# Optimization experiments

Hardware: AMD Instinct MI355X
Metric: run time of the kernel (lower is better)

Reference implementation:

```python
import jax, jax.numpy as jnp
import numpy as np

EPS = 1e-5
K = 3
N_TAP = K * K


def _bn(x, g, b, m, v):
    # eval-mode batchnorm over channel axis 1 of NCHW
    inv = g / jnp.sqrt(v + EPS)
    return x * inv[None, :, None, None] + (b - m * inv)[None, :, None, None]


def _silu(x):
    return x * jax.nn.sigmoid(x)


def _dcn(x, offset, mask, w, b, pad=1):
    """Modulated deformable conv (DCNv2), stride 1.
    x: [B,C,H,W], offset: [B,2n,H,W] ((dy,dx) per tap), mask: [B,n,H,W],
    w: [O,C,K,K], b: [O]."""
    B, C, H, W = x.shape
    O = w.shape[0]
    ky, kx = jnp.meshgrid(jnp.arange(K), jnp.arange(K), indexing='ij')
    ky = ky.reshape(N_TAP).astype(x.dtype)
    kx = kx.reshape(N_TAP).astype(x.dtype)
    off = offset.reshape(B, N_TAP, 2, H, W)
    base_y = jnp.arange(H, dtype=x.dtype)[None, None, :, None]
    base_x = jnp.arange(W, dtype=x.dtype)[None, None, None, :]
    # fractional sample positions [B,n,H,W]
    py = base_y - pad + ky[None, :, None, None] + off[:, :, 0]
    px = base_x - pad + kx[None, :, None, None] + off[:, :, 1]
    y0 = jnp.floor(py)
    x0 = jnp.floor(px)
    fy = py - y0
    fx = px - x0
    y0i = y0.astype(jnp.int32)
    x0i = x0.astype(jnp.int32)
    x_flat = x.reshape(B, C, 1, H * W)

    def corner(yi, xi, wgt):
        valid = (yi >= 0) & (yi < H) & (xi >= 0) & (xi < W)
        idx = (jnp.clip(yi, 0, H - 1) * W + jnp.clip(xi, 0, W - 1)).reshape(B, 1, N_TAP, H * W)
        v = jnp.take_along_axis(x_flat, idx, axis=-1)  # [B,C,n,HW]
        return v * (wgt * valid.astype(x.dtype)).reshape(B, 1, N_TAP, H * W)

    acc = corner(y0i, x0i, (1 - fy) * (1 - fx))
    acc = acc + corner(y0i, x0i + 1, (1 - fy) * fx)
    acc = acc + corner(y0i + 1, x0i, fy * (1 - fx))
    acc = acc + corner(y0i + 1, x0i + 1, fy * fx)
    val = acc.reshape(B, C, N_TAP, H, W) * mask[:, None]  # modulation
    out = jnp.einsum('bcnhw,ocn->bohw', val, w.reshape(O, C, N_TAP))
    return out + b[None, :, None, None]


def setup_inputs() -> dict:
    key = jax.random.key(0)
    ks = jax.random.split(key, 16)
    B, C1, H, W = 8, 256, 80, 80
    C2 = 256
    Ch = 128  # c_ = int(c2 * 0.5)
    d = {}
    d['x'] = jax.random.normal(ks[0], (B, C1, H, W), jnp.float32)
    # cv1: 1x1 conv (no bias) + BN
    d['cv1_w'] = jax.random.normal(ks[1], (Ch, C1), jnp.float32) * (1.0 / np.sqrt(C1))
    d['bn1_g'] = jax.random.uniform(ks[2], (Ch,), jnp.float32, 0.5, 1.5)
    d['bn1_b'] = jax.random.normal(ks[3], (Ch,), jnp.float32) * 0.1
    d['bn1_m'] = jax.random.normal(ks[4], (Ch,), jnp.float32) * 0.1
    d['bn1_v'] = jax.random.uniform(ks[5], (Ch,), jnp.float32, 0.5, 1.5)
    # offset/mask predictor 3x3 conv (small weights -> modest deformation)
    d['off_w'] = jax.random.normal(ks[6], (3 * N_TAP, Ch, K, K), jnp.float32) * 0.01
    d['off_b'] = jnp.zeros((3 * N_TAP,), jnp.float32)
    # dcn main weight/bias
    d['dcn_w'] = jax.random.normal(ks[7], (Ch, Ch, K, K), jnp.float32) * (1.0 / np.sqrt(Ch * N_TAP))
    d['dcn_b'] = jnp.zeros((Ch,), jnp.float32)
    d['bn2_g'] = jax.random.uniform(ks[8], (Ch,), jnp.float32, 0.5, 1.5)
    d['bn2_b'] = jax.random.normal(ks[9], (Ch,), jnp.float32) * 0.1
    d['bn2_m'] = jax.random.normal(ks[10], (Ch,), jnp.float32) * 0.1
    d['bn2_v'] = jax.random.uniform(ks[11], (Ch,), jnp.float32, 0.5, 1.5)
    # cv2: 1x1 conv (no bias) + BN
    d['cv2_w'] = jax.random.normal(ks[12], (C2, Ch), jnp.float32) * (1.0 / np.sqrt(Ch))
    d['bn3_g'] = jax.random.uniform(ks[13], (C2,), jnp.float32, 0.5, 1.5)
    d['bn3_b'] = jax.random.normal(ks[14], (C2,), jnp.float32) * 0.1
    d['bn3_m'] = jax.random.normal(ks[15], (C2,), jnp.float32) * 0.1
    d['bn3_v'] = jnp.ones((C2,), jnp.float32)
    return d


def reference(x, cv1_w, bn1_g, bn1_b, bn1_m, bn1_v,
              off_w, off_b, dcn_w, dcn_b, bn2_g, bn2_b, bn2_m, bn2_v,
              cv2_w, bn3_g, bn3_b, bn3_m, bn3_v):
    # cv1: 1x1 conv -> BN -> SiLU
    y = _silu(_bn(jnp.einsum('bchw,oc->bohw', x, cv1_w), bn1_g, bn1_b, bn1_m, bn1_v))
    # offset/mask predictor: 3x3 conv, pad 1
    raw = jax.lax.conv_general_dilated(
        y, off_w, window_strides=(1, 1), padding=((1, 1), (1, 1)),
        dimension_numbers=('NCHW', 'OIHW', 'NCHW')) + off_b[None, :, None, None]
    offset = raw[:, :2 * N_TAP]
    mask = jax.nn.sigmoid(raw[:, 2 * N_TAP:])
    # modulated deformable 3x3 conv -> BN -> SiLU
    y = _silu(_bn(_dcn(y, offset, mask, dcn_w, dcn_b), bn2_g, bn2_b, bn2_m, bn2_v))
    # cv2: 1x1 conv -> BN -> SiLU
    y = _silu(_bn(jnp.einsum('bchw,oc->bohw', y, cv2_w), bn3_g, bn3_b, bn3_m, bn3_v))
    return x + y  # shortcut (c1 == c2)
```

## Files before the change

kernel.cpp:

```cpp
#include <hip/hip_runtime.h>
#include <math.h>

#define HWSZ 6400
#define WIMG 80
#define HIMG 80
#define BEPS 1e-5f

typedef __attribute__((ext_vector_type(8))) short short8;
typedef __attribute__((ext_vector_type(4))) float f32x4;
typedef __attribute__((ext_vector_type(4))) unsigned u32x4;

__device__ __forceinline__ unsigned short f2b(float f) {
    unsigned u = __builtin_bit_cast(unsigned, f);
    u += 0x7fffu + ((u >> 16) & 1u);
    return (unsigned short)(u >> 16);
}
__device__ __forceinline__ float silu_f(float t) { return t / (1.f + __expf(-t)); }

#define BMFMA(a, b, c) __builtin_amdgcn_mfma_f32_16x16x32_bf16(a, b, c, 0, 0, 0)

__device__ __forceinline__ void gload16(const unsigned short* g, unsigned short* l) {
    __builtin_amdgcn_global_load_lds(
        (const __attribute__((address_space(1))) unsigned int*)g,
        (__attribute__((address_space(3))) unsigned int*)l, 16, 0, 0);
}

__global__ __launch_bounds__(256) void k_prep(
    const float* __restrict__ cv1w, const float* __restrict__ g1, const float* __restrict__ b1,
    const float* __restrict__ m1, const float* __restrict__ v1,
    const float* __restrict__ offw, const float* __restrict__ offb,
    const float* __restrict__ dcnw, const float* __restrict__ dcnb,
    const float* __restrict__ g2, const float* __restrict__ b2,
    const float* __restrict__ m2, const float* __restrict__ v2,
    const float* __restrict__ cv2w, const float* __restrict__ g3, const float* __restrict__ b3,
    const float* __restrict__ m3, const float* __restrict__ v3,
    unsigned short* __restrict__ apk1, unsigned short* __restrict__ apko,
    unsigned short* __restrict__ apkd, unsigned short* __restrict__ apk2,
    float* __restrict__ bias1, float* __restrict__ biaso,
    float* __restrict__ bias2, float* __restrict__ bias3)
{
    int idx = blockIdx.x * 256 + threadIdx.x;
    if (idx < 32768) {
        int j = idx & 7, L = (idx >> 3) & 63, ks = (idx >> 9) & 7, mt = idx >> 12;
        int o = mt * 16 + (L & 15), k = ks * 32 + (L >> 4) * 8 + j;
        float inv = g1[o] * rsqrtf(v1[o] + BEPS);
        apk1[idx] = f2b(cv1w[o * 256 + k] * inv);
    } else if (idx < 69632) {
        int t = idx - 32768;
        int j = t & 7, L = (t >> 3) & 63;
        int mt = t / 18432, rem = t % 18432, ks = rem >> 9;
        int o = mt * 16 + (L & 15);
        int kp = ks * 32 + (L >> 4) * 8 + j;
        int n = kp >> 7, c = kp & 127;
        float wv = (o < 27) ? offw[(size_t)(o * 128 + c) * 9 + n] : 0.f;
        apko[((size_t)(ks * 2 + mt) * 64 + L) * 8 + j] = f2b(wv);
    } else if (idx < 217088) {
        int t = idx - 69632;
        int j = t & 7, L = (t >> 3) & 63;
        int mt = t / 18432, rem = t % 18432, ks = rem >> 9;
        int o = mt * 16 + (L & 15);
        int kp = ks * 32 + (L >> 4) * 8 + j;
        int n = kp >> 7, c = kp & 127;
        float inv = g2[o] * rsqrtf(v2[o] + BEPS);
        apkd[((size_t)(ks * 8 + mt) * 64 + L) * 8 + j] = f2b(dcnw[(size_t)(o * 128 + c) * 9 + n] * inv);
    } else if (idx < 249856) {
        int t = idx - 217088;
        int j = t & 7, L = (t >> 3) & 63, ks = (t >> 9) & 3, mt = t >> 11;
        int o = mt * 16 + (L & 15), k = ks * 32 + (L >> 4) * 8 + j;
        float inv = g3[o] * rsqrtf(v3[o] + BEPS);
        apk2[((size_t)(ks * 16 + mt) * 64 + L) * 8 + j] = f2b(cv2w[o * 128 + k] * inv);
    } else if (idx < 250395) {
        int t = idx - 249856;
        if (t < 128) { float inv = g1[t] * rsqrtf(v1[t] + BEPS); bias1[t] = b1[t] - m1[t] * inv; }
        else if (t < 155) { biaso[t - 128] = offb[t - 128]; }
        else if (t < 283) { int o = t - 155; float inv = g2[o] * rsqrtf(v2[o] + BEPS);
                            bias2[o] = dcnb[o] * inv + b2[o] - m2[o] * inv; }
        else { int o = t - 283; float inv = g3[o] * rsqrtf(v3[o] + BEPS); bias3[o] = b3[o] - m3[o] * inv; }
    }
}

__global__ __launch_bounds__(256) void k_cv1(
    const float* __restrict__ x, const unsigned short* __restrict__ apk1,
    const float* __restrict__ bias1, unsigned short* __restrict__ y1t)
{
    __shared__ __align__(16) unsigned short sB[20480];
    int blk = blockIdx.x;
    int b = blk / 100, pt = blk % 100;
    int p0 = pt * 64;
    int tid = threadIdx.x;
    int lane = tid & 63;
    int w = tid >> 6;
    {
        int px = lane, q = w;
        const float* xb = x + (size_t)b * 256 * HWSZ + p0 + px;
        for (int ks = 0; ks < 8; ++ks) {
            unsigned pk[4];
#pragma unroll
            for (int t = 0; t < 4; ++t) {
                float f0 = xb[(size_t)(ks * 32 + q * 8 + 2 * t) * HWSZ];
                float f1 = xb[(size_t)(ks * 32 + q * 8 + 2 * t + 1) * HWSZ];
                asm("v_cvt_pk_bf16_f32 %0, %1, %2" : "=v"(pk[t]) : "v"(f0), "v"(f1));
            }
            *(u32x4*)&sB[((ks * 4 + (px >> 4)) * 16 + (px & 15)) * 40 + q * 8] =
                (u32x4){pk[0], pk[1], pk[2], pk[3]};
        }
    }
    __syncthreads();
    int n16 = lane & 15, qd = lane >> 4;
    f32x4 acc[2][4];
#pragma unroll
    for (int mi = 0; mi < 2; ++mi)
#pragma unroll
        for (int nt = 0; nt < 4; ++nt) acc[mi][nt] = (f32x4){0.f, 0.f, 0.f, 0.f};
    for (int ks = 0; ks < 8; ++ks) {
        short8 bf[4];
#pragma unroll
        for (int nt = 0; nt < 4; ++nt)
            bf[nt] = *(const short8*)&sB[((ks * 4 + nt) * 16 + n16) * 40 + qd * 8];
        short8 a0 = *(const short8*)&apk1[(size_t)(((w * 2 + 0) * 8 + ks) * 64 + lane) * 8];
        short8 a1 = *(const short8*)&apk1[(size_t)(((w * 2 + 1) * 8 + ks) * 64 + lane) * 8];
#pragma unroll
        for (int nt = 0; nt < 4; ++nt) acc[0][nt] = BMFMA(a0, bf[nt], acc[0][nt]);
#pragma unroll
        for (int nt = 0; nt < 4; ++nt) acc[1][nt] = BMFMA(a1, bf[nt], acc[1][nt]);
    }
    __syncthreads();
#pragma unroll
    for (int mi = 0; mi < 2; ++mi)
#pragma unroll
        for (int nt = 0; nt < 4; ++nt)
#pragma unroll
            for (int r = 0; r < 4; ++r) {
                int o = w * 32 + mi * 16 + qd * 4 + r;
                float sv = silu_f(acc[mi][nt][r] + bias1[o]);
                sB[(nt * 16 + n16) * 136 + o] = f2b(sv);
            }
    __syncthreads();
    {
        int px = tid >> 2, qq = tid & 3;
        unsigned short* ytb = y1t + ((size_t)b * HWSZ + p0 + px) * 128;
#pragma unroll
        for (int seg = 0; seg < 4; ++seg) {
            short8 v = *(const short8*)&sB[px * 136 + qq * 32 + seg * 8];
            *(short8*)&ytb[qq * 32 + seg * 8] = v;
        }
    }
}

#define HY2 8
#define HX2 20
#define NH 160
#define NSLAB 53

#define ACC8(uu, cb)                                                                   \
    {                                                                                  \
        _Pragma("unroll") for (int t = 0; t < 4; ++t) {                                \
            unsigned uv = (uu)[t];                                                     \
            av[(cb) + 2 * t] = fmaf(wk, __builtin_bit_cast(float, uv << 16),           \
                                    av[(cb) + 2 * t]);                                 \
            av[(cb) + 2 * t + 1] = fmaf(wk, __builtin_bit_cast(float, uv & 0xffff0000u),\
                                        av[(cb) + 2 * t + 1]);                         \
        }                                                                              \
    }

__device__ __forceinline__ const unsigned short* slab_src(
    const unsigned short* apko, const unsigned short* apkd,
    const unsigned short* apk2, int i) {
    if (i < 9)  return apko + (size_t)i * 4096;
    if (i < 45) return apkd + (size_t)(i - 9) * 4096;
    return apk2 + (size_t)(i - 45) * 4096;
}

#define STAGE(i, bp)                                                                   \
    {                                                                                  \
        const unsigned short* src_ = slab_src(apko, apkd, apk2, (i));                  \
        gload16(src_ + ((w * 2 + 0) * 512 + lane * 8), &sAf[bp][(w * 2 + 0) * 512]);   \
        gload16(src_ + ((w * 2 + 1) * 512 + lane * 8), &sAf[bp][(w * 2 + 1) * 512]);   \
    }

__global__ __launch_bounds__(256, 2) void k_odc(
    const unsigned short* __restrict__ y1t,
    const unsigned short* __restrict__ apko, const float* __restrict__ biaso,
    const unsigned short* __restrict__ apkd, const float* __restrict__ bias2,
    const unsigned short* __restrict__ apk2, const float* __restrict__ bias3,
    const float* __restrict__ x, float* __restrict__ out)
{
    __shared__ __align__(16) unsigned short sH[NH * 128];
    __shared__ float sRaw[27 * 66];
    __shared__ __align__(16) unsigned short sAf[2][4096];

    int blk = blockIdx.x;
    int b = blk / 100, pt = blk % 100;
    int h0 = (pt / 5) * 4, w0 = (pt % 5) * 16;
    int tid = threadIdx.x, lane = tid & 63, w = tid >> 6;
    int n16 = lane & 15, qd = lane >> 4;
    int pxl = w * 16 + n16;
    const unsigned short* yb = y1t + (size_t)b * HWSZ * 128;

    for (int i = tid; i < NH * 16; i += 256) {
        int r = i >> 4, u = i & 15;
        int ly = r / HX2, lx = r % HX2;
        int yy = min(max(h0 + ly - 2, 0), HIMG - 1);
        int xx = min(max(w0 + lx - 2, 0), WIMG - 1);
        *(u32x4*)&sH[r * 128 + ((u ^ (r & 7)) * 8)] =
            *(const u32x4*)&yb[(size_t)(yy * WIMG + xx) * 128 + u * 8];
    }
    STAGE(0, 0)
    __syncthreads();
    int bufp = 0;

    {
        f32x4 oa0 = (f32x4){0.f, 0.f, 0.f, 0.f};
        f32x4 oa1 = (f32x4){0.f, 0.f, 0.f, 0.f};
        for (int n = 0; n < 9; ++n) {
            STAGE(n + 1, bufp ^ 1)
            int dh = n / 3 - 1, dw = n % 3 - 1;
            int hh = h0 + w + dh, ww = w0 + n16 + dw;
            bool valid = ((unsigned)hh < HIMG) && ((unsigned)ww < WIMG);
            int r = (w + 2 + dh) * HX2 + (n16 + 2 + dw);
            int xr = r & 7;
            const unsigned short* hb = &sH[r * 128];
#pragma unroll
            for (int s = 0; s < 4; ++s) {
                short8 bf = *(const short8*)&hb[((s * 4 + qd) ^ xr) * 8];
                if (!valid) bf = (short8){0, 0, 0, 0, 0, 0, 0, 0};
                short8 a0 = *(const short8*)&sAf[bufp][(s * 2 + 0) * 512 + lane * 8];
                short8 a1 = *(const short8*)&sAf[bufp][(s * 2 + 1) * 512 + lane * 8];
                oa0 = BMFMA(a0, bf, oa0);
                oa1 = BMFMA(a1, bf, oa1);
            }
            if (n == 8) {
#pragma unroll
                for (int mi = 0; mi < 2; ++mi)
#pragma unroll
                    for (int r4 = 0; r4 < 4; ++r4) {
                        int o = mi * 16 + qd * 4 + r4;
                        if (o < 27) {
                            float t = (mi ? oa1[r4] : oa0[r4]) + biaso[o];
                            if (o >= 18) t = 1.f / (1.f + __expf(-t));
                            sRaw[o * 66 + pxl] = t;
                        }
                    }
            }
            __syncthreads();
            bufp ^= 1;
        }
    }

    f32x4 acc[8];
#pragma unroll
    for (int mt = 0; mt < 8; ++mt) acc[mt] = (f32x4){0.f, 0.f, 0.f, 0.f};
    int hI = h0 + w, wI = w0 + n16;

    for (int n = 0; n < 9; ++n) {
        float av[32];
#pragma unroll
        for (int s = 0; s < 4; ++s) {
            int slab = 9 + n * 4 + s;
            if (slab + 1 < NSLAB) STAGE(slab + 1, bufp ^ 1)
            if (s == 0) {
                float dy = sRaw[(2 * n) * 66 + pxl];
                float dx = sRaw[(2 * n + 1) * 66 + pxl];
                float mk = sRaw[(18 + n) * 66 + pxl];
                float py = (float)(hI - 1 + n / 3) + dy;
                float px = (float)(wI - 1 + n % 3) + dx;
                float y0f = floorf(py), x0f = floorf(px);
                float fy = py - y0f, fxv = px - x0f;
                int y0 = (int)y0f, x0 = (int)x0f;
                float wy0 = (1.f - fy) * mk, wy1 = fy * mk, fx1 = 1.f - fxv;
#pragma unroll
                for (int j = 0; j < 32; ++j) av[j] = 0.f;
#pragma unroll
                for (int k = 0; k < 4; ++k) {
                    int yy = y0 + (k >> 1), xx = x0 + (k & 1);
                    bool vld = ((unsigned)yy < HIMG) && ((unsigned)xx < WIMG);
                    float wk = ((k >> 1) ? wy1 : wy0) * ((k & 1) ? fxv : fx1);
                    if (!vld) wk = 0.f;
                    int yc = min(max(yy, 0), HIMG - 1);
                    int xc = min(max(xx, 0), WIMG - 1);
                    int ly = yc - h0 + 2, lx = xc - w0 + 2;
                    if (((unsigned)ly < HY2) && ((unsigned)lx < HX2)) {
                        int r = ly * HX2 + lx;
                        const unsigned short* hb = &sH[r * 128];
                        int xr = r & 7;
                        u32x4 u0 = *(const u32x4*)&hb[((0 + qd) ^ xr) * 8];
                        u32x4 u1 = *(const u32x4*)&hb[((4 + qd) ^ xr) * 8];
                        u32x4 u2 = *(const u32x4*)&hb[((8 + qd) ^ xr) * 8];
                        u32x4 u3 = *(const u32x4*)&hb[((12 + qd) ^ xr) * 8];
                        ACC8(u0, 0) ACC8(u1, 8) ACC8(u2, 16) ACC8(u3, 24)
                    } else if (wk != 0.f) {
                        const unsigned short* src = &yb[(size_t)(yc * WIMG + xc) * 128 + qd * 8];
                        u32x4 u0 = *(const u32x4*)src;
                        u32x4 u1 = *(const u32x4*)(src + 32);
                        u32x4 u2 = *(const u32x4*)(src + 64);
                        u32x4 u3 = *(const u32x4*)(src + 96);
                        ACC8(u0, 0) ACC8(u1, 8) ACC8(u2, 16) ACC8(u3, 24)
                    }
                }
            }
            unsigned pk0, pk1, pk2, pk3;
            asm("v_cvt_pk_bf16_f32 %0, %1, %2" : "=v"(pk0) : "v"(av[s * 8 + 0]), "v"(av[s * 8 + 1]));
            asm("v_cvt_pk_bf16_f32 %0, %1, %2" : "=v"(pk1) : "v"(av[s * 8 + 2]), "v"(av[s * 8 + 3]));
            asm("v_cvt_pk_bf16_f32 %0, %1, %2" : "=v"(pk2) : "v"(av[s * 8 + 4]), "v"(av[s * 8 + 5]));
            asm("v_cvt_pk_bf16_f32 %0, %1, %2" : "=v"(pk3) : "v"(av[s * 8 + 6]), "v"(av[s * 8 + 7]));
            short8 bfv = __builtin_bit_cast(short8, (u32x4){pk0, pk1, pk2, pk3});
#pragma unroll
            for (int mt = 0; mt < 8; ++mt) {
                short8 af = *(const short8*)&sAf[bufp][mt * 512 + lane * 8];
                acc[mt] = BMFMA(af, bfv, acc[mt]);
            }
            if (n == 8 && s == 3) {
                unsigned short* sE = sH;
#pragma unroll
                for (int mt = 0; mt < 8; ++mt)
#pragma unroll
                    for (int r4 = 0; r4 < 4; ++r4) {
                        int o = mt * 16 + qd * 4 + r4;
                        float sv = silu_f(acc[mt][r4] + bias2[o]);
                        sE[pxl * 136 + o] = f2b(sv);
                    }
            }
            __syncthreads();
            bufp ^= 1;
        }
    }

    const unsigned short* sE = sH;
    f32x4 c2[16];
#pragma unroll
    for (int mt = 0; mt < 16; ++mt) c2[mt] = (f32x4){0.f, 0.f, 0.f, 0.f};
#pragma unroll
    for (int h2 = 0; h2 < 8; ++h2) {
        int slab = 45 + h2;
        if (slab + 1 < NSLAB) STAGE(slab + 1, bufp ^ 1)
        int ks = h2 >> 1, half = h2 & 1;
        short8 bf = *(const short8*)&sE[pxl * 136 + ks * 32 + qd * 8];
#pragma unroll
        for (int mt = 0; mt < 8; ++mt) {
            short8 af = *(const short8*)&sAf[bufp][mt * 512 + lane * 8];
            c2[half * 8 + mt] = BMFMA(af, bf, c2[half * 8 + mt]);
        }
        __syncthreads();
        bufp ^= 1;
    }
    int p = (h0 + w) * WIMG + w0 + n16;
    const float* xb = x + (size_t)b * 256 * HWSZ;
    float* ob = out + (size_t)b * 256 * HWSZ;
#pragma unroll
    for (int mt = 0; mt < 16; ++mt)
#pragma unroll
        for (int r4 = 0; r4 < 4; ++r4) {
            int o = mt * 16 + qd * 4 + r4;
            size_t idx = (size_t)o * HWSZ + p;
            ob[idx] = xb[idx] + silu_f(c2[mt][r4] + bias3[o]);
        }
}

extern "C" void kernel_launch(void* const* d_in, const int* in_sizes, int n_in,
                              void* d_out, int out_size, void* d_ws, size_t ws_size,
                              hipStream_t stream) {
    const float* x     = (const float*)d_in[0];
    const float* cv1w  = (const float*)d_in[1];
    const float* bn1g  = (const float*)d_in[2];
    const float* bn1b  = (const float*)d_in[3];
    const float* bn1m  = (const float*)d_in[4];
    const float* bn1v  = (const float*)d_in[5];
    const float* offw  = (const float*)d_in[6];
    const float* offb  = (const float*)d_in[7];
    const float* dcnw  = (const float*)d_in[8];
    const float* dcnb  = (const float*)d_in[9];
    const float* bn2g  = (const float*)d_in[10];
    const float* bn2b  = (const float*)d_in[11];
    const float* bn2m  = (const float*)d_in[12];
    const float* bn2v  = (const float*)d_in[13];
    const float* cv2w  = (const float*)d_in[14];
    const float* bn3g  = (const float*)d_in[15];
    const float* bn3b  = (const float*)d_in[16];
    const float* bn3m  = (const float*)d_in[17];
    const float* bn3v  = (const float*)d_in[18];
    float* out = (float*)d_out;

    float* base = (float*)d_ws;
    unsigned short* y1t = (unsigned short*)base;
    unsigned short* apk1 = (unsigned short*)(base + 7936000);
    unsigned short* apko = (unsigned short*)(base + 7952384);
    unsigned short* apkd = (unsigned short*)(base + 7970816);
    unsigned short* apk2 = (unsigned short*)(base + 8044544);
    float* bias1 = base + 8060928;
    float* biaso = base + 8061056;
    float* bias2 = base + 8061088;
    float* bias3 = base + 8061216;

    k_prep<<<979, 256, 0, stream>>>(cv1w, bn1g, bn1b, bn1m, bn1v,
                                    offw, offb, dcnw, dcnb,
                                    bn2g, bn2b, bn2m, bn2v,
                                    cv2w, bn3g, bn3b, bn3m, bn3v,
                                    apk1, apko, apkd, apk2,
                                    bias1, biaso, bias2, bias3);
    k_cv1<<<800, 256, 0, stream>>>(x, apk1, bias1, y1t);
    k_odc<<<800, 256, 0, stream>>>(y1t, apko, biaso, apkd, bias2,
                                   apk2, bias3, x, out);
}
```

Before: 235.1 us.

## Drop LDS halo tile in fused offset/DCN kernel and raise occupancy to four blocks

```diff
diff --git a/kernel.cpp b/kernel.cpp
--- a/kernel.cpp
+++ b/kernel.cpp
@@ -112,13 +112,14 @@
     for (int mi = 0; mi < 2; ++mi)
 #pragma unroll
         for (int nt = 0; nt < 4; ++nt) acc[mi][nt] = (f32x4){0.f, 0.f, 0.f, 0.f};
+#pragma unroll
     for (int ks = 0; ks < 8; ++ks) {
+        short8 a0 = *(const short8*)&apk1[(size_t)(((w * 2 + 0) * 8 + ks) * 64 + lane) * 8];
+        short8 a1 = *(const short8*)&apk1[(size_t)(((w * 2 + 1) * 8 + ks) * 64 + lane) * 8];
         short8 bf[4];
 #pragma unroll
         for (int nt = 0; nt < 4; ++nt)
             bf[nt] = *(const short8*)&sB[((ks * 4 + nt) * 16 + n16) * 40 + qd * 8];
-        short8 a0 = *(const short8*)&apk1[(size_t)(((w * 2 + 0) * 8 + ks) * 64 + lane) * 8];
-        short8 a1 = *(const short8*)&apk1[(size_t)(((w * 2 + 1) * 8 + ks) * 64 + lane) * 8];
 #pragma unroll
         for (int nt = 0; nt < 4; ++nt) acc[0][nt] = BMFMA(a0, bf[nt], acc[0][nt]);
 #pragma unroll
@@ -147,9 +148,6 @@
     }
 }
 
-#define HY2 8
-#define HX2 20
-#define NH 160
 #define NSLAB 53
 
 #define ACC8(uu, cb)                                                                   \
@@ -178,16 +176,16 @@
         gload16(src_ + ((w * 2 + 1) * 512 + lane * 8), &sAf[bp][(w * 2 + 1) * 512]);   \
     }
 
-__global__ __launch_bounds__(256, 2) void k_odc(
+__global__ __launch_bounds__(256, 4) void k_odc(
     const unsigned short* __restrict__ y1t,
     const unsigned short* __restrict__ apko, const float* __restrict__ biaso,
     const unsigned short* __restrict__ apkd, const float* __restrict__ bias2,
     const unsigned short* __restrict__ apk2, const float* __restrict__ bias3,
     const float* __restrict__ x, float* __restrict__ out)
 {
-    __shared__ __align__(16) unsigned short sH[NH * 128];
     __shared__ float sRaw[27 * 66];
     __shared__ __align__(16) unsigned short sAf[2][4096];
+    __shared__ __align__(16) unsigned short sZ[64 * 132];
 
     int blk = blockIdx.x;
     int b = blk / 100, pt = blk % 100;
@@ -197,14 +195,6 @@
     int pxl = w * 16 + n16;
     const unsigned short* yb = y1t + (size_t)b * HWSZ * 128;
 
-    for (int i = tid; i < NH * 16; i += 256) {
-        int r = i >> 4, u = i & 15;
-        int ly = r / HX2, lx = r % HX2;
-        int yy = min(max(h0 + ly - 2, 0), HIMG - 1);
-        int xx = min(max(w0 + lx - 2, 0), WIMG - 1);
-        *(u32x4*)&sH[r * 128 + ((u ^ (r & 7)) * 8)] =
-            *(const u32x4*)&yb[(size_t)(yy * WIMG + xx) * 128 + u * 8];
-    }
     STAGE(0, 0)
     __syncthreads();
     int bufp = 0;
@@ -217,17 +207,21 @@
             int dh = n / 3 - 1, dw = n % 3 - 1;
             int hh = h0 + w + dh, ww = w0 + n16 + dw;
             bool valid = ((unsigned)hh < HIMG) && ((unsigned)ww < WIMG);
-            int r = (w + 2 + dh) * HX2 + (n16 + 2 + dw);
-            int xr = r & 7;
-            const unsigned short* hb = &sH[r * 128];
+            int row = min(max(hh, 0), HIMG - 1) * WIMG + min(max(ww, 0), WIMG - 1);
+            const unsigned short* ys = &yb[(size_t)row * 128 + qd * 8];
+            short8 bfv[4];
 #pragma unroll
             for (int s = 0; s < 4; ++s) {
-                short8 bf = *(const short8*)&hb[((s * 4 + qd) ^ xr) * 8];
-                if (!valid) bf = (short8){0, 0, 0, 0, 0, 0, 0, 0};
+                short8 v = *(const short8*)&ys[s * 32];
+                if (!valid) v = (short8){0, 0, 0, 0, 0, 0, 0, 0};
+                bfv[s] = v;
+            }
+#pragma unroll
+            for (int s = 0; s < 4; ++s) {
                 short8 a0 = *(const short8*)&sAf[bufp][(s * 2 + 0) * 512 + lane * 8];
                 short8 a1 = *(const short8*)&sAf[bufp][(s * 2 + 1) * 512 + lane * 8];
-                oa0 = BMFMA(a0, bf, oa0);
-                oa1 = BMFMA(a1, bf, oa1);
+                oa0 = BMFMA(a0, bfv[s], oa0);
+                oa1 = BMFMA(a1, bfv[s], oa1);
             }
             if (n == 8) {
 #pragma unroll
@@ -278,24 +272,12 @@
                     if (!vld) wk = 0.f;
                     int yc = min(max(yy, 0), HIMG - 1);
                     int xc = min(max(xx, 0), WIMG - 1);
-                    int ly = yc - h0 + 2, lx = xc - w0 + 2;
-                    if (((unsigned)ly < HY2) && ((unsigned)lx < HX2)) {
-                        int r = ly * HX2 + lx;
-                        const unsigned short* hb = &sH[r * 128];
-                        int xr = r & 7;
-                        u32x4 u0 = *(const u32x4*)&hb[((0 + qd) ^ xr) * 8];
-                        u32x4 u1 = *(const u32x4*)&hb[((4 + qd) ^ xr) * 8];
-                        u32x4 u2 = *(const u32x4*)&hb[((8 + qd) ^ xr) * 8];
-                        u32x4 u3 = *(const u32x4*)&hb[((12 + qd) ^ xr) * 8];
-                        ACC8(u0, 0) ACC8(u1, 8) ACC8(u2, 16) ACC8(u3, 24)
-                    } else if (wk != 0.f) {
-                        const unsigned short* src = &yb[(size_t)(yc * WIMG + xc) * 128 + qd * 8];
-                        u32x4 u0 = *(const u32x4*)src;
-                        u32x4 u1 = *(const u32x4*)(src + 32);
-                        u32x4 u2 = *(const u32x4*)(src + 64);
-                        u32x4 u3 = *(const u32x4*)(src + 96);
-                        ACC8(u0, 0) ACC8(u1, 8) ACC8(u2, 16) ACC8(u3, 24)
-                    }
+                    const unsigned short* src = &yb[(size_t)(yc * WIMG + xc) * 128 + qd * 8];
+                    u32x4 u0 = *(const u32x4*)src;
+                    u32x4 u1 = *(const u32x4*)(src + 32);
+                    u32x4 u2 = *(const u32x4*)(src + 64);
+                    u32x4 u3 = *(const u32x4*)(src + 96);
+                    ACC8(u0, 0) ACC8(u1, 8) ACC8(u2, 16) ACC8(u3, 24)
                 }
             }
             unsigned pk0, pk1, pk2, pk3;
@@ -310,14 +292,13 @@
                 acc[mt] = BMFMA(af, bfv, acc[mt]);
             }
             if (n == 8 && s == 3) {
-                unsigned short* sE = sH;
 #pragma unroll
                 for (int mt = 0; mt < 8; ++mt)
 #pragma unroll
                     for (int r4 = 0; r4 < 4; ++r4) {
                         int o = mt * 16 + qd * 4 + r4;
                         float sv = silu_f(acc[mt][r4] + bias2[o]);
-                        sE[pxl * 136 + o] = f2b(sv);
+                        sZ[pxl * 132 + o] = f2b(sv);
                     }
             }
             __syncthreads();
@@ -325,7 +306,6 @@
         }
     }
 
-    const unsigned short* sE = sH;
     f32x4 c2[16];
 #pragma unroll
     for (int mt = 0; mt < 16; ++mt) c2[mt] = (f32x4){0.f, 0.f, 0.f, 0.f};
@@ -334,7 +314,7 @@
         int slab = 45 + h2;
         if (slab + 1 < NSLAB) STAGE(slab + 1, bufp ^ 1)
         int ks = h2 >> 1, half = h2 & 1;
-        short8 bf = *(const short8*)&sE[pxl * 136 + ks * 32 + qd * 8];
+        short8 bf = *(const short8*)&sZ[pxl * 132 + ks * 32 + qd * 8];
 #pragma unroll
         for (int mt = 0; mt < 8; ++mt) {
             short8 af = *(const short8*)&sAf[bufp][mt * 512 + lane * 8];
```

New measurement: 248.0 us. +5.5%, slower.
